# Optimization experiments

Measured on AMD Instinct MI355X. Metric: run time of the kernel, lower is better.

Reference implementation:

```python
import jax, jax.numpy as jnp
import numpy as np

B, T, H = 8, 2048, 1024

def setup_inputs() -> dict:
    key = jax.random.key(0)
    ks = jax.random.split(key, 7)
    s = 1.0 / np.sqrt(H)
    return {
        "x": jax.random.normal(ks[0], (B, T, H), dtype=jnp.float32),
        "Wq": jax.random.uniform(ks[1], (H, H), jnp.float32, -s, s),
        "bq": jax.random.uniform(ks[2], (H,), jnp.float32, -s, s),
        "Wk": jax.random.uniform(ks[3], (H, H), jnp.float32, -s, s),
        "bk": jax.random.uniform(ks[4], (H,), jnp.float32, -s, s),
        "Wv": jax.random.uniform(ks[5], (H, H), jnp.float32, -s, s),
        "bv": jax.random.uniform(ks[6], (H,), jnp.float32, -s, s),
    }

def reference(x, Wq, bq, Wk, bk, Wv, bv):
    # Linear layers: y = x @ W^T + b (torch convention: store W as [out,in]; here square so use [in,out] directly)
    Q = x @ Wq + bq                      # [B, T, H]
    K = x @ Wk + bk
    V = x @ Wv + bv
    scores = jnp.einsum('bqd,bkd->bqk', Q, K) / jnp.sqrt(jnp.float32(x.shape[-1]))
    # NOTE: original uses nn.Softmax(dim=1) -> softmax over the QUERY axis (axis=1)
    attention = jax.nn.softmax(scores, axis=1)  # [B, T, T]
    out = jnp.einsum('bqk,bkd->bqd', attention, V)
    return out
```

## Files before the change

kernel.cpp:

```cpp
#include <hip/hip_runtime.h>
#include <hip/hip_bf16.h>

typedef __attribute__((ext_vector_type(8))) short short8;
typedef __attribute__((ext_vector_type(4))) float f32x4;

__device__ __forceinline__ float bf2f(unsigned short u) {
    unsigned v = ((unsigned)u) << 16;
    float f;
    __builtin_memcpy(&f, &v, 4);
    return f;
}
__device__ __forceinline__ unsigned short f2bf(float f) {
    unsigned v;
    __builtin_memcpy(&v, &f, 4);
    unsigned r = (v + 0x7fffu + ((v >> 16) & 1u)) >> 16;
    return (unsigned short)r;
}

#define GLD16(g, l)                                                            \
    __builtin_amdgcn_global_load_lds(                                          \
        (const __attribute__((address_space(1))) void*)(g),                    \
        (__attribute__((address_space(3))) void*)(l), 16, 0, 0)

__global__ __launch_bounds__(256) void cast_f32_bf16(const float* __restrict__ in,
                                                     unsigned short* __restrict__ out,
                                                     size_t n) {
    size_t stride = (size_t)gridDim.x * blockDim.x * 4;
    for (size_t i = ((size_t)blockIdx.x * blockDim.x + threadIdx.x) * 4; i < n; i += stride) {
        float4 v = *(const float4*)(in + i);
        ushort4 o;
        o.x = f2bf(v.x); o.y = f2bf(v.y); o.z = f2bf(v.z); o.w = f2bf(v.w);
        *(ushort4*)(out + i) = o;
    }
}

__global__ __launch_bounds__(256) void cast_transpose_w(const float* __restrict__ W,
                                                        unsigned short* __restrict__ WT, int D) {
    __shared__ float tile[32][33];
    int bx = blockIdx.x * 32;
    int by = blockIdx.y * 32;
    int tx = threadIdx.x & 31, ty = threadIdx.x >> 5;
    for (int i = 0; i < 32; i += 8)
        tile[ty + i][tx] = W[(size_t)(by + ty + i) * D + bx + tx];
    __syncthreads();
    for (int i = 0; i < 32; i += 8)
        WT[(size_t)(bx + ty + i) * D + by + tx] = f2bf(tile[tx][ty + i]);
}

__global__ __launch_bounds__(256) void concat3(const float* __restrict__ a,
                                               const float* __restrict__ b,
                                               const float* __restrict__ c,
                                               float* __restrict__ o, int n) {
    int i = blockIdx.x * 256 + threadIdx.x;
    if (i < n) { o[i] = a[i]; o[n + i] = b[i]; o[2 * n + i] = c[i]; }
}

template <int EPI>
__global__ __launch_bounds__(512, 2) void gemm256(
    const unsigned short* __restrict__ A, const unsigned short* __restrict__ B,
    void* __restrict__ Cv, const float* __restrict__ bias,
    int K, float scale, int lda, int ldb, int ldc,
    long sA, long sB, long sC) {
    __shared__ __attribute__((aligned(16))) unsigned short sm[2][2][2][8192];

    const int tid = threadIdx.x;
    const int wv = tid >> 6, lane = tid & 63;
    const int wm = wv >> 2, wn = wv & 3;
    const int r16 = lane & 15, cHi = lane >> 4;
    const int tileM = blockIdx.y * 256, tileN = blockIdx.x * 256;
    const int bz = blockIdx.z;
    A += (size_t)bz * sA;
    B += (size_t)bz * sB;

    size_t offA[2], offB[2];
    int ldsOff[2];
    const int swzsrc = ((lane & 3) ^ ((lane >> 3) & 3)) * 8;
#pragma unroll
    for (int j = 0; j < 2; ++j) {
        int row = (wv * 2 + j) * 16 + (lane >> 2);
        offA[j] = (size_t)(tileM + row) * lda + swzsrc;
        offB[j] = (size_t)(tileN + row) * ldb + swzsrc;
        ldsOff[j] = (wv * 2 + j) * 1024;
    }

#define STAGE(BUF, P, KT)                                                       \
    do {                                                                        \
        const unsigned short* _s = ((P) & 1) ? B : A;                           \
        const size_t* _o = ((P) & 1) ? offB : offA;                             \
        char* _d = (char*)&sm[BUF][(P) >> 1][(P) & 1][0];                       \
        GLD16(_s + _o[0] + (KT) + ((P) >> 1) * 32, _d + ldsOff[0]);             \
        GLD16(_s + _o[1] + (KT) + ((P) >> 1) * 32, _d + ldsOff[1]);             \
    } while (0)

    f32x4 acc[8][4];
#pragma unroll
    for (int m = 0; m < 8; ++m)
#pragma unroll
        for (int n = 0; n < 4; ++n) acc[m][n] = (f32x4){0.f, 0.f, 0.f, 0.f};

    const int slotXor = (lane >> 1) & 3;
    const int aBase = (wm * 128 + r16) * 32 + (cHi ^ slotXor) * 8;
    const int bBase = (wn * 64 + r16) * 32 + (cHi ^ slotXor) * 8;

    STAGE(0, 0, 0); STAGE(0, 1, 0); STAGE(0, 2, 0); STAGE(0, 3, 0);
    asm volatile("s_waitcnt vmcnt(4)" ::: "memory");
    __builtin_amdgcn_s_barrier();

    short8 aF[8], bF0, bF1;
    const int nt = K >> 6;
    for (int t = 0; t < nt; ++t) {
        const int cur = t & 1, nxt = cur ^ 1;
        const int ktn = (t + 1 == nt) ? 0 : ((t + 1) << 6);
        const unsigned short* A0 = &sm[cur][0][0][0];
        const unsigned short* B0 = &sm[cur][0][1][0];
        const unsigned short* A1 = &sm[cur][1][0][0];
        const unsigned short* B1 = &sm[cur][1][1][0];

#pragma unroll
        for (int m = 0; m < 8; ++m) aF[m] = *(const short8*)&A0[aBase + m * 512];
        bF0 = *(const short8*)&B0[bBase];
        bF1 = *(const short8*)&B0[bBase + 512];
        STAGE(nxt, 0, ktn);
        __builtin_amdgcn_s_barrier();
        asm volatile("s_waitcnt lgkmcnt(0)" ::: "memory");
        __builtin_amdgcn_sched_barrier(0);
        __builtin_amdgcn_s_setprio(1);
#pragma unroll
        for (int m = 0; m < 8; ++m) {
            acc[m][0] = __builtin_amdgcn_mfma_f32_16x16x32_bf16(aF[m], bF0, acc[m][0], 0, 0, 0);
            acc[m][1] = __builtin_amdgcn_mfma_f32_16x16x32_bf16(aF[m], bF1, acc[m][1], 0, 0, 0);
        }
        __builtin_amdgcn_s_setprio(0);
        __builtin_amdgcn_s_barrier();

        bF0 = *(const short8*)&B0[bBase + 1024];
        bF1 = *(const short8*)&B0[bBase + 1536];
        STAGE(nxt, 1, ktn);
        __builtin_amdgcn_s_barrier();
        asm volatile("s_waitcnt lgkmcnt(0)" ::: "memory");
        __builtin_amdgcn_sched_barrier(0);
        __builtin_amdgcn_s_setprio(1);
#pragma unroll
        for (int m = 0; m < 8; ++m) {
            acc[m][2] = __builtin_amdgcn_mfma_f32_16x16x32_bf16(aF[m], bF0, acc[m][2], 0, 0, 0);
            acc[m][3] = __builtin_amdgcn_mfma_f32_16x16x32_bf16(aF[m], bF1, acc[m][3], 0, 0, 0);
        }
        __builtin_amdgcn_s_setprio(0);
        asm volatile("s_waitcnt vmcnt(4)" ::: "memory");
        __builtin_amdgcn_s_barrier();

#pragma unroll
        for (int m = 0; m < 8; ++m) aF[m] = *(const short8*)&A1[aBase + m * 512];
        bF0 = *(const short8*)&B1[bBase];
        bF1 = *(const short8*)&B1[bBase + 512];
        STAGE(nxt, 2, ktn);
        __builtin_amdgcn_s_barrier();
        asm volatile("s_waitcnt lgkmcnt(0)" ::: "memory");
        __builtin_amdgcn_sched_barrier(0);
        __builtin_amdgcn_s_setprio(1);
#pragma unroll
        for (int m = 0; m < 8; ++m) {
            acc[m][0] = __builtin_amdgcn_mfma_f32_16x16x32_bf16(aF[m], bF0, acc[m][0], 0, 0, 0);
            acc[m][1] = __builtin_amdgcn_mfma_f32_16x16x32_bf16(aF[m], bF1, acc[m][1], 0, 0, 0);
        }
        __builtin_amdgcn_s_setprio(0);
        __builtin_amdgcn_s_barrier();

        bF0 = *(const short8*)&B1[bBase + 1024];
        bF1 = *(const short8*)&B1[bBase + 1536];
        STAGE(nxt, 3, ktn);
        __builtin_amdgcn_s_barrier();
        asm volatile("s_waitcnt lgkmcnt(0)" ::: "memory");
        __builtin_amdgcn_sched_barrier(0);
        __builtin_amdgcn_s_setprio(1);
#pragma unroll
        for (int m = 0; m < 8; ++m) {
            acc[m][2] = __builtin_amdgcn_mfma_f32_16x16x32_bf16(aF[m], bF0, acc[m][2], 0, 0, 0);
            acc[m][3] = __builtin_amdgcn_mfma_f32_16x16x32_bf16(aF[m], bF1, acc[m][3], 0, 0, 0);
        }
        __builtin_amdgcn_s_setprio(0);
        asm volatile("s_waitcnt vmcnt(4)" ::: "memory");
        __builtin_amdgcn_s_barrier();
    }
    asm volatile("s_waitcnt vmcnt(0)" ::: "memory");
#undef STAGE

    const int rowB = tileM + wm * 128 + cHi * 4;
    const int colB = tileN + wn * 64 + r16;
#pragma unroll
    for (int m = 0; m < 8; ++m) {
#pragma unroll
        for (int n = 0; n < 4; ++n) {
            const int col = colB + n * 16;
            float badd = (EPI == 0) ? bias[col] : 0.f;
#pragma unroll
            for (int r = 0; r < 4; ++r) {
                int row = rowB + m * 16 + r;
                float v = acc[m][n][r];
                if (EPI == 0) v += badd;
                if (EPI == 1) v = __expf(v * scale);
                size_t idx = (size_t)bz * sC + (size_t)row * ldc + col;
                if (EPI == 2) ((float*)Cv)[idx] = v;
                else ((unsigned short*)Cv)[idx] = f2bf(v);
            }
        }
    }
}

__global__ __launch_bounds__(256) void col_sum_partial(const unsigned short* __restrict__ E,
                                                       float* __restrict__ partial, int T) {
    int b = blockIdx.z;
    int k = blockIdx.x * 256 + threadIdx.x;
    int q0 = blockIdx.y * 64;
    const unsigned short* p = E + (size_t)b * T * T + (size_t)q0 * T + k;
    float sum = 0.f;
#pragma unroll 4
    for (int q = 0; q < 64; ++q)
        sum += bf2f(p[(size_t)q * T]);
    partial[((size_t)b * gridDim.y + blockIdx.y) * T + k] = sum;
}

__global__ __launch_bounds__(256) void col_sum_reduce(const float* __restrict__ partial,
                                                      float* __restrict__ invl, int T, int nchunk) {
    int b = blockIdx.y;
    int k = blockIdx.x * 256 + threadIdx.x;
    float s = 0.f;
    for (int c = 0; c < nchunk; ++c)
        s += partial[((size_t)b * nchunk + c) * T + k];
    invl[(size_t)b * T + k] = 1.0f / s;
}

__global__ __launch_bounds__(256) void transpose_scale_bf16(
    const unsigned short* __restrict__ V, const float* __restrict__ invl,
    unsigned short* __restrict__ Vt, int T, int H, int ldv) {
    __shared__ unsigned short tile[64][66];
    int b = blockIdx.z;
    const unsigned short* Vb = V + (size_t)b * T * ldv;
    unsigned short* Vtb = Vt + (size_t)b * H * T;
    const float* il = invl + (size_t)b * T;
    int x0 = blockIdx.x * 64;
    int y0 = blockIdx.y * 64;
    int t = threadIdx.x;
    for (int i = 0; i < 16; ++i) {
        int idx = t + i * 256;
        int r = idx >> 6, c = idx & 63;
        tile[r][c] = Vb[(size_t)(y0 + r) * ldv + x0 + c];
    }
    __syncthreads();
    for (int i = 0; i < 16; ++i) {
        int idx = t + i * 256;
        int r = idx >> 6, c = idx & 63;
        float v = bf2f(tile[c][r]) * il[y0 + c];
        Vtb[(size_t)(x0 + r) * T + y0 + c] = f2bf(v);
    }
}

extern "C" void kernel_launch(void* const* d_in, const int* in_sizes, int n_in,
                              void* d_out, int out_size, void* d_ws, size_t ws_size,
                              hipStream_t stream) {
    const int B = 8, T = 2048, H = 1024;
    const size_t MT = (size_t)B * T;
    const int H3 = 3 * H;

    const float* x  = (const float*)d_in[0];
    const float* Wq = (const float*)d_in[1];
    const float* bq = (const float*)d_in[2];
    const float* Wk = (const float*)d_in[3];
    const float* bk = (const float*)d_in[4];
    const float* Wv = (const float*)d_in[5];
    const float* bv = (const float*)d_in[6];
    float* out = (float*)d_out;

    char* ws = (char*)d_ws;
    size_t o = 0;
    unsigned short* xb   = (unsigned short*)(ws + o); o += MT * H * 2;
    unsigned short* Wcat = (unsigned short*)(ws + o); o += (size_t)H3 * H * 2;
    float* bcat          = (float*)(ws + o);          o += (size_t)H3 * 4;
    unsigned short* QKVb = (unsigned short*)(ws + o); o += MT * H3 * 2;
    unsigned short* Eb   = (unsigned short*)(ws + o); o += (size_t)B * T * T * 2;
    float* partial       = (float*)(ws + o);          o += (size_t)B * 32 * T * 4;
    float* invl          = (float*)(ws + o);          o += (size_t)B * T * 4;
    unsigned short* Vt   = xb;

    cast_f32_bf16<<<2048, 256, 0, stream>>>(x, xb, MT * H);
    dim3 wgrid(32, 32);
    cast_transpose_w<<<wgrid, 256, 0, stream>>>(Wq, Wcat, H);
    cast_transpose_w<<<wgrid, 256, 0, stream>>>(Wk, Wcat + (size_t)H * H, H);
    cast_transpose_w<<<wgrid, 256, 0, stream>>>(Wv, Wcat + (size_t)2 * H * H, H);
    concat3<<<4, 256, 0, stream>>>(bq, bk, bv, bcat, H);

    gemm256<0><<<dim3(H3 / 256, MT / 256, 1), 512, 0, stream>>>(
        xb, Wcat, QKVb, bcat, H, 1.f, H, H, H3, 0, 0, 0);

    gemm256<1><<<dim3(T / 256, T / 256, B), 512, 0, stream>>>(
        QKVb, QKVb + H, Eb, nullptr, H, 0.03125f, H3, H3, T,
        (long)T * H3, (long)T * H3, (long)T * T);

    col_sum_partial<<<dim3(T / 256, 32, B), 256, 0, stream>>>(Eb, partial, T);
    col_sum_reduce<<<dim3(T / 256, B), 256, 0, stream>>>(partial, invl, T, 32);

    transpose_scale_bf16<<<dim3(H / 64, T / 64, B), 256, 0, stream>>>(
        QKVb + 2 * H, invl, Vt, T, H, H3);

    gemm256<2><<<dim3(H / 256, T / 256, B), 512, 0, stream>>>(
        Eb, Vt, out, nullptr, T, 1.f, T, T, H,
        (long)T * T, (long)H * T, (long)T * H);

    (void)in_sizes; (void)n_in; (void)out_size; (void)ws_size;
}
```

Before: 320.8 us.

## Restructure GEMM main loop into a 4-slot ring with 3-deep prefetch

Replaces the double-buffered 64-wide K tile loop, which had four sub-phases and many barriers, with a 4-slot ring of 32-wide K slices. Loads for slice H+3 are issued while slice H is computed, and each iteration has a single barrier and 32 MFMAs with all B fragments loaded up front. The aim is to keep more global loads in flight and cut barrier overhead. In exchange, each iteration holds more registers for fragments, and ring reuse depends on the vmcnt accounting being right.

```diff
diff --git a/kernel.cpp b/kernel.cpp
--- a/kernel.cpp
+++ b/kernel.cpp
@@ -83,13 +83,13 @@
         ldsOff[j] = (wv * 2 + j) * 1024;
     }
 
-#define STAGE(BUF, P, KT)                                                       \
+#define STAGE_OP(OP, S, KT)                                                     \
     do {                                                                        \
-        const unsigned short* _s = ((P) & 1) ? B : A;                           \
-        const size_t* _o = ((P) & 1) ? offB : offA;                             \
-        char* _d = (char*)&sm[BUF][(P) >> 1][(P) & 1][0];                       \
-        GLD16(_s + _o[0] + (KT) + ((P) >> 1) * 32, _d + ldsOff[0]);             \
-        GLD16(_s + _o[1] + (KT) + ((P) >> 1) * 32, _d + ldsOff[1]);             \
+        const unsigned short* _s = (OP) ? B : A;                                \
+        const size_t* _o = (OP) ? offB : offA;                                  \
+        char* _d = (char*)&sm[((S) >> 1) & 1][(S) & 1][OP][0];                  \
+        GLD16(_s + _o[0] + (KT), _d + ldsOff[0]);                               \
+        GLD16(_s + _o[1] + (KT), _d + ldsOff[1]);                               \
     } while (0)
 
     f32x4 acc[8][4];
@@ -102,88 +102,43 @@
     const int aBase = (wm * 128 + r16) * 32 + (cHi ^ slotXor) * 8;
     const int bBase = (wn * 64 + r16) * 32 + (cHi ^ slotXor) * 8;
 
-    STAGE(0, 0, 0); STAGE(0, 1, 0); STAGE(0, 2, 0); STAGE(0, 3, 0);
-    asm volatile("s_waitcnt vmcnt(4)" ::: "memory");
+    STAGE_OP(0, 0, 0); STAGE_OP(1, 0, 0);
+    STAGE_OP(0, 1, 32); STAGE_OP(1, 1, 32);
+    STAGE_OP(0, 2, 64); STAGE_OP(1, 2, 64);
+    asm volatile("s_waitcnt vmcnt(8)" ::: "memory");
     __builtin_amdgcn_s_barrier();
 
-    short8 aF[8], bF0, bF1;
-    const int nt = K >> 6;
-    for (int t = 0; t < nt; ++t) {
-        const int cur = t & 1, nxt = cur ^ 1;
-        const int ktn = (t + 1 == nt) ? 0 : ((t + 1) << 6);
-        const unsigned short* A0 = &sm[cur][0][0][0];
-        const unsigned short* B0 = &sm[cur][0][1][0];
-        const unsigned short* A1 = &sm[cur][1][0][0];
-        const unsigned short* B1 = &sm[cur][1][1][0];
-
-#pragma unroll
-        for (int m = 0; m < 8; ++m) aF[m] = *(const short8*)&A0[aBase + m * 512];
-        bF0 = *(const short8*)&B0[bBase];
-        bF1 = *(const short8*)&B0[bBase + 512];
-        STAGE(nxt, 0, ktn);
-        __builtin_amdgcn_s_barrier();
+    const int nslot = K >> 5;
+    for (int H = 0; H < nslot; ++H) {
+        const unsigned short* Abuf = &sm[(H >> 1) & 1][H & 1][0][0];
+        const unsigned short* Bbuf = &sm[(H >> 1) & 1][H & 1][1][0];
+
+        short8 aF[8], bF[4];
+#pragma unroll
+        for (int m = 0; m < 8; ++m) aF[m] = *(const short8*)&Abuf[aBase + m * 512];
+#pragma unroll
+        for (int n = 0; n < 4; ++n) bF[n] = *(const short8*)&Bbuf[bBase + n * 512];
+
+        const int S = H + 3;
+        const int kt = ((S << 5) < K) ? (S << 5) : 0;
+        STAGE_OP(0, S, kt);
+        STAGE_OP(1, S, kt);
+
         asm volatile("s_waitcnt lgkmcnt(0)" ::: "memory");
         __builtin_amdgcn_sched_barrier(0);
         __builtin_amdgcn_s_setprio(1);
 #pragma unroll
         for (int m = 0; m < 8; ++m) {
-            acc[m][0] = __builtin_amdgcn_mfma_f32_16x16x32_bf16(aF[m], bF0, acc[m][0], 0, 0, 0);
-            acc[m][1] = __builtin_amdgcn_mfma_f32_16x16x32_bf16(aF[m], bF1, acc[m][1], 0, 0, 0);
+#pragma unroll
+            for (int n = 0; n < 4; ++n)
+                acc[m][n] = __builtin_amdgcn_mfma_f32_16x16x32_bf16(aF[m], bF[n], acc[m][n], 0, 0, 0);
         }
         __builtin_amdgcn_s_setprio(0);
+        asm volatile("s_waitcnt vmcnt(8)" ::: "memory");
         __builtin_amdgcn_s_barrier();
-
-        bF0 = *(const short8*)&B0[bBase + 1024];
-        bF1 = *(const short8*)&B0[bBase + 1536];
-        STAGE(nxt, 1, ktn);
-        __builtin_amdgcn_s_barrier();
-        asm volatile("s_waitcnt lgkmcnt(0)" ::: "memory");
-        __builtin_amdgcn_sched_barrier(0);
-        __builtin_amdgcn_s_setprio(1);
-#pragma unroll
-        for (int m = 0; m < 8; ++m) {
-            acc[m][2] = __builtin_amdgcn_mfma_f32_16x16x32_bf16(aF[m], bF0, acc[m][2], 0, 0, 0);
-            acc[m][3] = __builtin_amdgcn_mfma_f32_16x16x32_bf16(aF[m], bF1, acc[m][3], 0, 0, 0);
-        }
-        __builtin_amdgcn_s_setprio(0);
-        asm volatile("s_waitcnt vmcnt(4)" ::: "memory");
-        __builtin_amdgcn_s_barrier();
-
-#pragma unroll
-        for (int m = 0; m < 8; ++m) aF[m] = *(const short8*)&A1[aBase + m * 512];
-        bF0 = *(const short8*)&B1[bBase];
-        bF1 = *(const short8*)&B1[bBase + 512];
-        STAGE(nxt, 2, ktn);
-        __builtin_amdgcn_s_barrier();
-        asm volatile("s_waitcnt lgkmcnt(0)" ::: "memory");
-        __builtin_amdgcn_sched_barrier(0);
-        __builtin_amdgcn_s_setprio(1);
-#pragma unroll
-        for (int m = 0; m < 8; ++m) {
-            acc[m][0] = __builtin_amdgcn_mfma_f32_16x16x32_bf16(aF[m], bF0, acc[m][0], 0, 0, 0);
-            acc[m][1] = __builtin_amdgcn_mfma_f32_16x16x32_bf16(aF[m], bF1, acc[m][1], 0, 0, 0);
-        }
-        __builtin_amdgcn_s_setprio(0);
-        __builtin_amdgcn_s_barrier();
-
-        bF0 = *(const short8*)&B1[bBase + 1024];
-        bF1 = *(const short8*)&B1[bBase + 1536];
-        STAGE(nxt, 3, ktn);
-        __builtin_amdgcn_s_barrier();
-        asm volatile("s_waitcnt lgkmcnt(0)" ::: "memory");
-        __builtin_amdgcn_sched_barrier(0);
-        __builtin_amdgcn_s_setprio(1);
-#pragma unroll
-        for (int m = 0; m < 8; ++m) {
-            acc[m][2] = __builtin_amdgcn_mfma_f32_16x16x32_bf16(aF[m], bF0, acc[m][2], 0, 0, 0);
-            acc[m][3] = __builtin_amdgcn_mfma_f32_16x16x32_bf16(aF[m], bF1, acc[m][3], 0, 0, 0);
-        }
-        __builtin_amdgcn_s_setprio(0);
-        asm volatile("s_waitcnt vmcnt(4)" ::: "memory");
-        __builtin_amdgcn_s_barrier();
     }
     asm volatile("s_waitcnt vmcnt(0)" ::: "memory");
-#undef STAGE
+#undef STAGE_OP
 
     const int rowB = tileM + wm * 128 + cHi * 4;
     const int colB = tileN + wn * 64 + r16;
```

Result: no change. 326.9 us (+1.9%).
